# Optimization experiments

Hardware: AMD Instinct MI355X
Metric: run time of the kernel (lower is better)

Reference implementation:

```python
import jax, jax.numpy as jnp
import numpy as np

CELL = 512
DENSE = 2048
PRED = 24 * 24  # predict_ahead * 24
FEAT = 24
FORGET_BIAS = 1.0


def setup_inputs() -> dict:
    key = jax.random.key(0)
    ks = jax.random.split(key, 7)
    B, T = 1024, 512
    s = lambda fan_in: 1.0 / np.sqrt(fan_in)
    return {
        "X": jax.random.normal(ks[0], (B, T, FEAT), dtype=jnp.float32),
        "W_lstm": jax.random.normal(ks[1], (FEAT + CELL, 4 * CELL), dtype=jnp.float32) * s(FEAT + CELL),
        "b_lstm": jnp.zeros((4 * CELL,), dtype=jnp.float32),
        "W_dense": jax.random.normal(ks[2], (CELL, DENSE), dtype=jnp.float32) * s(CELL),
        "b_dense": jnp.zeros((DENSE,), dtype=jnp.float32),
        "W_pred": jax.random.normal(ks[3], (DENSE, PRED), dtype=jnp.float32) * s(DENSE),
        "b_pred": jnp.zeros((PRED,), dtype=jnp.float32),
    }


def reference(X, W_lstm, b_lstm, W_dense, b_dense, W_pred, b_pred):
    B = X.shape[0]
    c0 = jnp.zeros((B, CELL), dtype=X.dtype)
    h0 = jnp.zeros((B, CELL), dtype=X.dtype)

    def step(carry, x_t):
        c, h = carry
        z = jnp.concatenate([x_t, h], axis=1) @ W_lstm + b_lstm  # [B, 4*CELL]
        i, j, f, o = jnp.split(z, 4, axis=1)  # TF BasicLSTMCell gate order
        new_c = c * jax.nn.sigmoid(f + FORGET_BIAS) + jax.nn.sigmoid(i) * jnp.tanh(j)
        new_h = jnp.tanh(new_c) * jax.nn.sigmoid(o)
        return (new_c, new_h), None

    xs = jnp.swapaxes(X, 0, 1)  # [T, B, FEAT]
    (c_T, h_T), _ = jax.lax.scan(step, (c0, h0), xs)
    dense = jax.nn.relu(h_T @ W_dense + b_dense)
    preds = dense @ W_pred + b_pred
    return preds
```

## Files before the change

### kernel.cpp

```cpp
#include <hip/hip_runtime.h>
#include <hip/hip_fp16.h>

#define BATCH 1024
#define SEQ 512
#define NFEAT 24
#define NCELL 512
#define ZC 2048
#define KP 544
#define NCH 17
#define KL 576
#define DENSE_N 2048
#define PRED_N 576
#define NWG 256
#define NGRP 16
#define GWG 16
#define PFD 6
#define NBUF 7

typedef unsigned short u16;
typedef unsigned int u32;
typedef unsigned long long u64;
typedef unsigned short u16x8 __attribute__((ext_vector_type(8)));
typedef _Float16 f16x8 __attribute__((ext_vector_type(8)));
typedef float f32x4 __attribute__((ext_vector_type(4)));

__device__ __forceinline__ float sigm(float x) { return 1.f / (1.f + __expf(-x)); }
__device__ __forceinline__ float ftanh(float x) {
    float t = __expf(-2.f * fabsf(x));
    float r = (1.f - t) / (1.f + t);
    return copysignf(r, x);
}
__device__ __forceinline__ u16 f2h(float v) {
    _Float16 h = (_Float16)v;
    return *(u16*)&h;
}
__device__ __forceinline__ void st16(u16* p, u32 v) {
    asm volatile("global_store_short %0, %1, off sc0 sc1" :: "v"(p), "v"(v) : "memory");
}
__device__ __forceinline__ void st128(u16* p, u16x8 v) {
    asm volatile("global_store_dwordx4 %0, %1, off sc0 sc1" :: "v"(p), "v"(v) : "memory");
}

__device__ __forceinline__ u32 hword16(int row, int k) {
    int g = row >> 6, w = (row >> 4) & 3, r = row & 15;
    int ch = k >> 5, kk = k & 31;
    return (u32)(((g * 4 + w) * NCH + ch) * 512)
         + (u32)(((r | ((kk >> 3) << 4)) << 3) + (kk & 7));
}

__global__ __launch_bounds__(256) void prep_w(const float* __restrict__ W,
                                              u16* __restrict__ Wt) {
    int o = blockIdx.x * 256 + threadIdx.x;
    if (o >= ZC * KP) return;
    int n = o / KP, k = o % KP;
    float v = 0.f;
    if (k < NCELL)              v = W[(size_t)(NFEAT + k) * ZC + n];
    else if (k < NCELL + NFEAT) v = W[(size_t)(k - NCELL) * ZC + n];
    Wt[o] = f2h(v);
}

__global__ __launch_bounds__(256) void prep_h(const float* __restrict__ X,
                                              u16* __restrict__ H0, u16* __restrict__ H1) {
    int o = blockIdx.x * 256 + threadIdx.x;
    if (o >= BATCH * KP) return;
    int row = o / KP, k = o % KP;
    u16 b = 0;
    if (k >= NCELL && k < NCELL + NFEAT)
        b = f2h(X[(size_t)row * (SEQ * NFEAT) + (k - NCELL)]);
    u32 w = hword16(row, k);
    H0[w] = b;
    H1[w] = 0;
}

__global__ __launch_bounds__(256, 1) void lstm_persist(
    u16* __restrict__ H0, u16* __restrict__ H1,
    const u16* __restrict__ Wt,
    const float* __restrict__ bias,
    const float* __restrict__ X,
    float* __restrict__ hf32,
    int* __restrict__ bar)
{
    extern __shared__ u16 Ws[];

    const int tid = (int)threadIdx.x;
    const int bid = (int)blockIdx.x;
    const int g = bid & 15, nb2 = bid >> 4;
    const int r0 = g * 64;
    const int lane = tid & 63, wv = tid >> 6;
    u16* __restrict__ Hs = Ws + 128 * KL;
    int* __restrict__ bcnt   = bar + g * 64;
    int* __restrict__ bepoch = bar + g * 64 + 32;

    for (int e = tid; e < 128 * (KP / 8); e += 256) {
        int col = e / (KP / 8), k8 = (e % (KP / 8)) * 8;
        int n = col >> 4, cl = col & 15;
        int zc = (n & 3) * NCELL + nb2 * 32 + (n >> 2) * 16 + cl;
        int so = k8 ^ ((col & 7) << 3);
        *(u16x8*)&Ws[col * KL + so] = *(const u16x8*)&Wt[(size_t)zc * KP + k8];
    }
    __syncthreads();

    const int cell0 = nb2 * 32 + (lane & 15);
    const int cell1 = cell0 + 16;
    const float bi0 = bias[cell0],           bi1 = bias[cell1];
    const float bj0 = bias[NCELL + cell0],   bj1 = bias[NCELL + cell1];
    const float bf0 = bias[2*NCELL + cell0], bf1 = bias[2*NCELL + cell1];
    const float bo0 = bias[3*NCELL + cell0], bo1 = bias[3*NCELL + cell1];

    const int akof = (lane >> 4) * 8;
    const u32 abase = (u32)((g * 4 + wv) * NCH) * 128u + (u32)lane * 2u;

    const u32 esto = (u32)((g * 4 + wv) * NCH + nb2) * 512u + (u32)lane * 8u;
    const int hsw = (wv << 9);

    float ct[2][4] = {};

    for (int t = 0; t < SEQ; ++t) {
        const u64* Hq = (const u64*)((t & 1) ? H1 : H0);
        u16*       Np = (t & 1) ? H0 : H1;

        f32x4 acc[8] = {};
        __attribute__((aligned(16))) u64 fr[NBUF][2];

#define ALOADS(f, ch) do { \
        f[0] = __hip_atomic_load(&Hq[abase + (u32)(ch) * 128u],     __ATOMIC_RELAXED, __HIP_MEMORY_SCOPE_AGENT); \
        f[1] = __hip_atomic_load(&Hq[abase + (u32)(ch) * 128u + 1], __ATOMIC_RELAXED, __HIP_MEMORY_SCOPE_AGENT); \
        } while (0)
#define WSOFF(cb, off) ((cb) * KL + (((off)) ^ (((cb) & 7) << 3)))
#define CCOMP(f, ch) do { \
        f16x8 a = *(const f16x8*)&f[0]; \
        _Pragma("unroll") \
        for (int n = 0; n < 8; ++n) { \
            f16x8 bn = *(const f16x8*)&Ws[WSOFF(n * 16 + (lane & 15), (ch) * 32 + akof)]; \
            acc[n] = __builtin_amdgcn_mfma_f32_16x16x32_f16(a, bn, acc[n], 0, 0, 0); \
        } } while (0)

        ALOADS(fr[0], 0); ALOADS(fr[1], 1); ALOADS(fr[2], 2);
        ALOADS(fr[3], 3); ALOADS(fr[4], 4); ALOADS(fr[5], 5);
        #pragma unroll
        for (int ch = 0; ch < NCH; ++ch) {
            if (ch + PFD < NCH) ALOADS(fr[(ch + PFD) % NBUF], ch + PFD);
            CCOMP(fr[ch % NBUF], ch);
        }
#undef ALOADS
#undef CCOMP

        #pragma unroll
        for (int c2 = 0; c2 < 2; ++c2) {
            #pragma unroll
            for (int r = 0; r < 4; ++r) {
                int row16 = (lane >> 4) * 4 + r;
                float zi = acc[c2 * 4 + 0][r] + (c2 ? bi1 : bi0);
                float zj = acc[c2 * 4 + 1][r] + (c2 ? bj1 : bj0);
                float zf = acc[c2 * 4 + 2][r] + (c2 ? bf1 : bf0);
                float zo = acc[c2 * 4 + 3][r] + (c2 ? bo1 : bo0);
                float cn = ct[c2][r] * sigm(zf + 1.0f) + sigm(zi) * ftanh(zj);
                ct[c2][r] = cn;
                float h = ftanh(cn) * sigm(zo);
                Hs[hsw + ((row16 | ((c2 * 2 + ((lane >> 3) & 1)) << 4)) << 3) + (lane & 7)] = f2h(h);
                if (t == SEQ - 1) {
                    int row = r0 + wv * 16 + row16;
                    hf32[(size_t)row * NCELL + (c2 ? cell1 : cell0)] = h;
                }
            }
        }
        {
            u16x8 v = *(const u16x8*)&Hs[hsw + lane * 8];
            st128(&Np[esto], v);
        }
        if (t + 1 < SEQ && tid < 96) {
            int e = nb2 * 96 + tid;
            int rowg = e / 24, kk = e % 24;
            int row = r0 + rowg;
            float v = X[(size_t)row * (SEQ * NFEAT) + (t + 1) * NFEAT + kk];
            int w2 = rowg >> 4, r16 = rowg & 15;
            u32 idx = (u32)((g * 4 + w2) * NCH + 16) * 512u
                    + (u32)(((r16 | ((kk >> 3) << 4)) << 3) + (kk & 7));
            st16(&Np[idx], (u32)f2h(v));
        }

        __syncthreads();
        if (tid == 0) {
            int n = __hip_atomic_fetch_add(bcnt, 1, __ATOMIC_RELAXED, __HIP_MEMORY_SCOPE_AGENT);
            if (n == GWG - 1) {
                __hip_atomic_store(bcnt, 0, __ATOMIC_RELAXED, __HIP_MEMORY_SCOPE_AGENT);
                __hip_atomic_store(bepoch, t + 1, __ATOMIC_RELAXED, __HIP_MEMORY_SCOPE_AGENT);
            } else {
                int spins = 0;
                while (__hip_atomic_load(bepoch, __ATOMIC_RELAXED, __HIP_MEMORY_SCOPE_AGENT) <= t) {
                    __builtin_amdgcn_s_sleep(2);
                    if (++spins > 20000000) break;
                }
            }
        }
        __syncthreads();
    }
}

template <int ACT>
__global__ __launch_bounds__(256) void gemm64(
    const float* __restrict__ A, const float* __restrict__ Wm,
    const float* __restrict__ bias, float* __restrict__ out,
    int M, int N, int K)
{
    __shared__ float Asf[32][65];
    __shared__ float Bsf[32][65];
    const int c0 = blockIdx.x * 64;
    const int r0 = blockIdx.y * 64;
    const int tid = (int)threadIdx.x;
    const int tx = tid & 15, ty = tid >> 4;

    float acc[4][4];
    #pragma unroll
    for (int r = 0; r < 4; ++r) { acc[r][0]=0.f; acc[r][1]=0.f; acc[r][2]=0.f; acc[r][3]=0.f; }

    for (int k0 = 0; k0 < K; k0 += 32) {
        #pragma unroll
        for (int i = 0; i < 8; ++i) {
            int e = tid + 256 * i;
            int row = e >> 5, kk = e & 31;
            Asf[kk][row] = A[(size_t)(r0 + row) * K + k0 + kk];
        }
        #pragma unroll
        for (int i = 0; i < 8; ++i) {
            int e = tid + 256 * i;
            int kk = e >> 6, cl = e & 63;
            Bsf[kk][cl] = Wm[(size_t)(k0 + kk) * N + c0 + cl];
        }
        __syncthreads();
        #pragma unroll
        for (int kk = 0; kk < 32; ++kk) {
            float b0 = Bsf[kk][tx*4], b1 = Bsf[kk][tx*4+1], b2 = Bsf[kk][tx*4+2], b3 = Bsf[kk][tx*4+3];
            #pragma unroll
            for (int r = 0; r < 4; ++r) {
                float a = Asf[kk][ty*4 + r];
                acc[r][0] = fmaf(a, b0, acc[r][0]);
                acc[r][1] = fmaf(a, b1, acc[r][1]);
                acc[r][2] = fmaf(a, b2, acc[r][2]);
                acc[r][3] = fmaf(a, b3, acc[r][3]);
            }
        }
        __syncthreads();
    }
    #pragma unroll
    for (int r = 0; r < 4; ++r) {
        int gr = r0 + ty * 4 + r;
        #pragma unroll
        for (int j = 0; j < 4; ++j) {
            int gc = c0 + tx * 4 + j;
            float v = acc[r][j] + bias[gc];
            if (ACT) v = fmaxf(v, 0.f);
            out[(size_t)gr * N + gc] = v;
        }
    }
}

extern "C" void kernel_launch(void* const* d_in, const int* in_sizes, int n_in,
                              void* d_out, int out_size, void* d_ws, size_t ws_size,
                              hipStream_t stream)
{
    const float* X  = (const float*)d_in[0];
    const float* Wl = (const float*)d_in[1];
    const float* bl = (const float*)d_in[2];
    const float* Wd = (const float*)d_in[3];
    const float* bd = (const float*)d_in[4];
    const float* Wp = (const float*)d_in[5];
    const float* bp = (const float*)d_in[6];
    float* out = (float*)d_out;

    char* p = (char*)d_ws;
    int* bar      = (int*)p; p += 4096;
    float* hf32   = (float*)p; p += (size_t)BATCH * NCELL * 4;
    float* dense  = (float*)p; p += (size_t)BATCH * DENSE_N * 4;
    u16* Wt   = (u16*)p; p += (size_t)ZC * KP * 2;
    u16* H0   = (u16*)p; p += (size_t)BATCH * KP * 2;
    u16* H1   = (u16*)p; p += (size_t)BATCH * KP * 2;

    (void)hipMemsetAsync(bar, 0, 4096, stream);
    prep_w<<<(ZC * KP) / 256, 256, 0, stream>>>(Wl, Wt);
    prep_h<<<(BATCH * KP) / 256, 256, 0, stream>>>(X, H0, H1);

    const int lds_bytes = 128 * KL * 2 + 4 * 512 * 2;
    (void)hipFuncSetAttribute((const void*)lstm_persist,
                              hipFuncAttributeMaxDynamicSharedMemorySize, lds_bytes);
    lstm_persist<<<NWG, 256, lds_bytes, stream>>>(H0, H1, Wt, bl, X, hf32, bar);

    dim3 blk(256);
    gemm64<1><<<dim3(DENSE_N / 64, BATCH / 64), blk, 0, stream>>>(hf32, Wd, bd, dense, BATCH, DENSE_N, NCELL);
    gemm64<0><<<dim3(PRED_N / 64, BATCH / 64), blk, 0, stream>>>(dense, Wp, bp, out, BATCH, PRED_N, DENSE_N);
}
```

Before: 2.911 ms.

## Split LSTM workgroup into 8 waves, each handling half the gate columns

Doubles the persistent LSTM workgroup from 4 to 8 waves. Each pair of waves shares one 16-row block of H, and each wave computes one 16-cell half of the gate tile, so it issues 4 MFMAs per K-chunk instead of 8. This shortens the serial per-timestep critical path and halves the accumulator and register load per wave. In exchange, every H fragment is loaded from global memory twice (once per wave in the pair), stores narrow to 64-bit, and there are more waves to synchronise.

```diff
diff --git a/kernel.cpp b/kernel.cpp
--- a/kernel.cpp
+++ b/kernel.cpp
@@ -37,8 +37,8 @@
 __device__ __forceinline__ void st16(u16* p, u32 v) {
     asm volatile("global_store_short %0, %1, off sc0 sc1" :: "v"(p), "v"(v) : "memory");
 }
-__device__ __forceinline__ void st128(u16* p, u16x8 v) {
-    asm volatile("global_store_dwordx4 %0, %1, off sc0 sc1" :: "v"(p), "v"(v) : "memory");
+__device__ __forceinline__ void st64(u16* p, u64 v) {
+    asm volatile("global_store_dwordx2 %0, %1, off sc0 sc1" :: "v"(p), "v"(v) : "memory");
 }
 
 __device__ __forceinline__ u32 hword16(int row, int k) {
@@ -72,7 +72,7 @@
     H1[w] = 0;
 }
 
-__global__ __launch_bounds__(256, 1) void lstm_persist(
+__global__ __launch_bounds__(512, 1) void lstm_persist(
     u16* __restrict__ H0, u16* __restrict__ H1,
     const u16* __restrict__ Wt,
     const float* __restrict__ bias,
@@ -87,11 +87,12 @@
     const int g = bid & 15, nb2 = bid >> 4;
     const int r0 = g * 64;
     const int lane = tid & 63, wv = tid >> 6;
+    const int fi = wv >> 1, ci = wv & 1;
     u16* __restrict__ Hs = Ws + 128 * KL;
     int* __restrict__ bcnt   = bar + g * 64;
     int* __restrict__ bepoch = bar + g * 64 + 32;
 
-    for (int e = tid; e < 128 * (KP / 8); e += 256) {
+    for (int e = tid; e < 128 * (KP / 8); e += 512) {
         int col = e / (KP / 8), k8 = (e % (KP / 8)) * 8;
         int n = col >> 4, cl = col & 15;
         int zc = (n & 3) * NCELL + nb2 * 32 + (n >> 2) * 16 + cl;
@@ -100,39 +101,37 @@
     }
     __syncthreads();
 
-    const int cell0 = nb2 * 32 + (lane & 15);
-    const int cell1 = cell0 + 16;
-    const float bi0 = bias[cell0],           bi1 = bias[cell1];
-    const float bj0 = bias[NCELL + cell0],   bj1 = bias[NCELL + cell1];
-    const float bf0 = bias[2*NCELL + cell0], bf1 = bias[2*NCELL + cell1];
-    const float bo0 = bias[3*NCELL + cell0], bo1 = bias[3*NCELL + cell1];
+    const int cell = nb2 * 32 + ci * 16 + (lane & 15);
+    const float bi = bias[cell], bj = bias[NCELL + cell];
+    const float bf_ = bias[2 * NCELL + cell], bo = bias[3 * NCELL + cell];
 
     const int akof = (lane >> 4) * 8;
-    const u32 abase = (u32)((g * 4 + wv) * NCH) * 128u + (u32)lane * 2u;
-
-    const u32 esto = (u32)((g * 4 + wv) * NCH + nb2) * 512u + (u32)lane * 8u;
-    const int hsw = (wv << 9);
-
-    float ct[2][4] = {};
+    const u32 abase = (u32)((g * 4 + fi) * NCH) * 128u + (u32)lane * 2u;
+
+    const u32 esto = (u32)((g * 4 + fi) * NCH + nb2) * 512u + (u32)ci * 256u + (u32)lane * 4u;
+    const int hsw = (wv << 8);
+
+#define WSOFF(cb, off) ((cb) * KL + (((off)) ^ (((cb) & 7) << 3)))
+
+    float ct[4] = {};
 
     for (int t = 0; t < SEQ; ++t) {
         const u64* Hq = (const u64*)((t & 1) ? H1 : H0);
         u16*       Np = (t & 1) ? H0 : H1;
 
-        f32x4 acc[8] = {};
+        f32x4 acc[4] = {};
         __attribute__((aligned(16))) u64 fr[NBUF][2];
 
 #define ALOADS(f, ch) do { \
         f[0] = __hip_atomic_load(&Hq[abase + (u32)(ch) * 128u],     __ATOMIC_RELAXED, __HIP_MEMORY_SCOPE_AGENT); \
         f[1] = __hip_atomic_load(&Hq[abase + (u32)(ch) * 128u + 1], __ATOMIC_RELAXED, __HIP_MEMORY_SCOPE_AGENT); \
         } while (0)
-#define WSOFF(cb, off) ((cb) * KL + (((off)) ^ (((cb) & 7) << 3)))
 #define CCOMP(f, ch) do { \
         f16x8 a = *(const f16x8*)&f[0]; \
         _Pragma("unroll") \
-        for (int n = 0; n < 8; ++n) { \
-            f16x8 bn = *(const f16x8*)&Ws[WSOFF(n * 16 + (lane & 15), (ch) * 32 + akof)]; \
-            acc[n] = __builtin_amdgcn_mfma_f32_16x16x32_f16(a, bn, acc[n], 0, 0, 0); \
+        for (int gt = 0; gt < 4; ++gt) { \
+            f16x8 bn = *(const f16x8*)&Ws[WSOFF((ci * 4 + gt) * 16 + (lane & 15), (ch) * 32 + akof)]; \
+            acc[gt] = __builtin_amdgcn_mfma_f32_16x16x32_f16(a, bn, acc[gt], 0, 0, 0); \
         } } while (0)
 
         ALOADS(fr[0], 0); ALOADS(fr[1], 1); ALOADS(fr[2], 2);
@@ -146,27 +145,24 @@
 #undef CCOMP
 
         #pragma unroll
-        for (int c2 = 0; c2 < 2; ++c2) {
-            #pragma unroll
-            for (int r = 0; r < 4; ++r) {
-                int row16 = (lane >> 4) * 4 + r;
-                float zi = acc[c2 * 4 + 0][r] + (c2 ? bi1 : bi0);
-                float zj = acc[c2 * 4 + 1][r] + (c2 ? bj1 : bj0);
-                float zf = acc[c2 * 4 + 2][r] + (c2 ? bf1 : bf0);
-                float zo = acc[c2 * 4 + 3][r] + (c2 ? bo1 : bo0);
-                float cn = ct[c2][r] * sigm(zf + 1.0f) + sigm(zi) * ftanh(zj);
-                ct[c2][r] = cn;
-                float h = ftanh(cn) * sigm(zo);
-                Hs[hsw + ((row16 | ((c2 * 2 + ((lane >> 3) & 1)) << 4)) << 3) + (lane & 7)] = f2h(h);
-                if (t == SEQ - 1) {
-                    int row = r0 + wv * 16 + row16;
-                    hf32[(size_t)row * NCELL + (c2 ? cell1 : cell0)] = h;
-                }
+        for (int r = 0; r < 4; ++r) {
+            int row16 = (lane >> 4) * 4 + r;
+            float zi = acc[0][r] + bi;
+            float zj = acc[1][r] + bj;
+            float zf = acc[2][r] + bf_;
+            float zo = acc[3][r] + bo;
+            float cn = ct[r] * sigm(zf + 1.0f) + sigm(zi) * ftanh(zj);
+            ct[r] = cn;
+            float h = ftanh(cn) * sigm(zo);
+            Hs[hsw + ((row16 | (((lane >> 3) & 1) << 4)) << 3) + (lane & 7)] = f2h(h);
+            if (t == SEQ - 1) {
+                int row = r0 + fi * 16 + row16;
+                hf32[(size_t)row * NCELL + cell] = h;
             }
         }
         {
-            u16x8 v = *(const u16x8*)&Hs[hsw + lane * 8];
-            st128(&Np[esto], v);
+            u64 v = *(const u64*)&Hs[hsw + lane * 4];
+            st64(&Np[esto], v);
         }
         if (t + 1 < SEQ && tid < 96) {
             int e = nb2 * 96 + tid;
@@ -280,10 +276,10 @@
     prep_w<<<(ZC * KP) / 256, 256, 0, stream>>>(Wl, Wt);
     prep_h<<<(BATCH * KP) / 256, 256, 0, stream>>>(X, H0, H1);
 
-    const int lds_bytes = 128 * KL * 2 + 4 * 512 * 2;
+    const int lds_bytes = 128 * KL * 2 + 8 * 256 * 2;
     (void)hipFuncSetAttribute((const void*)lstm_persist,
                               hipFuncAttributeMaxDynamicSharedMemorySize, lds_bytes);
-    lstm_persist<<<NWG, 256, lds_bytes, stream>>>(H0, H1, Wt, bl, X, hf32, bar);
+    lstm_persist<<<NWG, 512, lds_bytes, stream>>>(H0, H1, Wt, bl, X, hf32, bar);
 
     dim3 blk(256);
     gemm64<1><<<dim3(DENSE_N / 64, BATCH / 64), blk, 0, stream>>>(hf32, Wd, bd, dense, BATCH, DENSE_N, NCELL);
```

New measurement: 2.704 ms, median of 2. -7.1%, faster.
